# Kernel tuning notes

Measured on AMD Instinct MI355X. Metric: run time of the kernel, lower is better.

## Reference

```python
import jax, jax.numpy as jnp
import numpy as np

IN0, OUT0 = 64, 64   # layer 0: input_size -> hidden
IN1, OUT1 = 64, 16   # layer 1: hidden -> output_size
H = 2                # subnetwork hidden width (subnetwork_shape=[2,2])
BATCH = 16384


def _make_layer_params(key, n_subnets):
    ks = jax.random.split(key, 6)
    s1 = 1.0  # fan_in=1
    s2 = 1.0 / np.sqrt(H)
    W1 = jax.random.uniform(ks[0], (n_subnets, H, 1), minval=-s1, maxval=s1)
    b1 = jax.random.uniform(ks[1], (n_subnets, H), minval=-s1, maxval=s1)
    W2 = jax.random.uniform(ks[2], (n_subnets, H, H), minval=-s2, maxval=s2)
    b2 = jax.random.uniform(ks[3], (n_subnets, H), minval=-s2, maxval=s2)
    W3 = jax.random.uniform(ks[4], (n_subnets, 1, H), minval=-s2, maxval=s2)
    b3 = jax.random.uniform(ks[5], (n_subnets, 1), minval=-s2, maxval=s2)
    return W1, b1, W2, b2, W3, b3


def setup_inputs() -> dict:
    key = jax.random.key(0)
    kx, k0, k1 = jax.random.split(key, 3)
    x = jax.random.normal(kx, (BATCH, IN0), dtype=jnp.float32)
    l0 = _make_layer_params(k0, IN0 * OUT0)
    l1 = _make_layer_params(k1, IN1 * OUT1)
    names = ['W1', 'b1', 'W2', 'b2', 'W3', 'b3']
    inp = {'x': x}
    for n, v in zip(names, l0):
        inp['l0_' + n] = v
    for n, v in zip(names, l1):
        inp['l1_' + n] = v
    return inp


def _kan_layer(x, in_size, out_size, W1, b1, W2, b2, W3, b3):
    # x: [B, in] -> x_expanded: [in*out, B, 1]; subnet n = i*out + o
    B = x.shape[0]
    xe = jnp.repeat(x.T, out_size, axis=0)[:, :, None]          # [N, B, 1]
    h = jax.nn.relu(jnp.einsum('nbi,nhi->nbh', xe, W1) + b1[:, None, :])  # [N, B, H]
    h = jax.nn.relu(jnp.einsum('nbh,nkh->nbk', h, W2) + b2[:, None, :])   # [N, B, H]
    o = jnp.einsum('nbk,nok->nbo', h, W3) + b3[:, None, :]                # [N, B, 1]
    o = o[..., 0].reshape(in_size, out_size, B).sum(axis=0)               # [out, B]
    return o.T                                                            # [B, out]


def reference(x, l0_W1, l0_b1, l0_W2, l0_b2, l0_W3, l0_b3,
              l1_W1, l1_b1, l1_W2, l1_b2, l1_W3, l1_b3):
    h = _kan_layer(x, IN0, OUT0, l0_W1, l0_b1, l0_W2, l0_b2, l0_W3, l0_b3)
    out = _kan_layer(h, IN1, OUT1, l1_W1, l1_b1, l1_W2, l1_b2, l1_W3, l1_b3)
    return out
```

## Files before the change

### kernel.cpp

```cpp
#include <hip/hip_runtime.h>


typedef float v2f __attribute__((ext_vector_type(2)));

#define BATCH 16384
#define TB    32

__global__ __launch_bounds__(512, 4) void kan_fused(
    const float* __restrict__ x,
    const float* __restrict__ A1, const float* __restrict__ a1,
    const float* __restrict__ A2, const float* __restrict__ a2,
    const float* __restrict__ A3, const float* __restrict__ a3,
    const float* __restrict__ B1, const float* __restrict__ c1,
    const float* __restrict__ B2, const float* __restrict__ c2,
    const float* __restrict__ B3, const float* __restrict__ c3,
    float* __restrict__ out)
{
    __shared__ float xs[64][36];
    __shared__ float hp[4][TB][64];
    __shared__ float ht[64][36];
    __shared__ float op[4][TB][16];

    const int t    = threadIdx.x;
    const int lane = t & 63;
    const int wave = t >> 6;
    const int iq   = wave & 3;
    const int bh   = wave >> 2;
    const int bB0  = blockIdx.x * TB;

    {
        const int k = t * 4;
        const float4 v = *(const float4*)(x + (long)bB0 * 64 + k);
        const int b = k >> 6, i = k & 63;
        xs[i][b] = v.x; xs[i + 1][b] = v.y; xs[i + 2][b] = v.z; xs[i + 3][b] = v.w;
    }
    __syncthreads();

    const v2f zz = {0.f, 0.f};
    const int boff = 16 * bh;

    {
        const int o  = lane;
        const int i0 = 16 * iq;

        auto ldw = [&](int i, v2f& w1, v2f& d1, float4& w2, v2f& d2, v2f& w3, float& b3v) {
            const int n = (i << 6) + o;
            w1  = *(const v2f*)(A1 + 2 * n);
            d1  = *(const v2f*)(a1 + 2 * n);
            w2  = *(const float4*)(A2 + 4 * n);
            d2  = *(const v2f*)(a2 + 2 * n);
            w3  = *(const v2f*)(A3 + 2 * n);
            b3v = a3[n];
        };

        v2f acc[8];
#pragma unroll
        for (int j = 0; j < 8; ++j) acc[j] = zz;
        float bsum = 0.f;

        v2f w1, d1, d2, w3; float4 w2; float b3v;
        ldw(i0, w1, d1, w2, d2, w3, b3v);

#pragma unroll 1
        for (int ii = 0; ii < 16; ++ii) {
            const int i = i0 + ii;
            v2f nw1, nd1, nd2, nw3; float4 nw2; float nb3;
            ldw(i0 + ((ii + 1) & 15), nw1, nd1, nw2, nd2, nw3, nb3);

            const v2f W1X = {w1.x, w1.x}, W1Y = {w1.y, w1.y};
            const v2f D1X = {d1.x, d1.x}, D1Y = {d1.y, d1.y};
            const v2f W2X = {w2.x, w2.x}, W2Y = {w2.y, w2.y};
            const v2f W2Z = {w2.z, w2.z}, W2W = {w2.w, w2.w};
            const v2f D2X = {d2.x, d2.x}, D2Y = {d2.y, d2.y};
            const v2f W3X = {w3.x, w3.x}, W3Y = {w3.y, w3.y};

            const float4 xv0 = *(const float4*)&xs[i][boff];
            const float4 xv1 = *(const float4*)&xs[i][boff + 4];
            const float4 xv2 = *(const float4*)&xs[i][boff + 8];
            const float4 xv3 = *(const float4*)&xs[i][boff + 12];
            const float4 xq[4] = {xv0, xv1, xv2, xv3};
            const v2f* xp = (const v2f*)xq;

            bsum += b3v;
#pragma unroll
            for (int jp = 0; jp < 8; ++jp) {
                v2f m0 = __builtin_elementwise_fma(xp[jp], W1X, D1X);
                v2f m1 = __builtin_elementwise_fma(xp[jp], W1Y, D1Y);
                m0 = __builtin_elementwise_max(m0, zz);
                m1 = __builtin_elementwise_max(m1, zz);
                v2f t0 = __builtin_elementwise_fma(W2Y, m1, D2X);
                t0 = __builtin_elementwise_fma(W2X, m0, t0);
                v2f t1 = __builtin_elementwise_fma(W2W, m1, D2Y);
                t1 = __builtin_elementwise_fma(W2Z, m0, t1);
                t0 = __builtin_elementwise_max(t0, zz);
                t1 = __builtin_elementwise_max(t1, zz);
                acc[jp] = __builtin_elementwise_fma(W3X, t0, acc[jp]);
                acc[jp] = __builtin_elementwise_fma(W3Y, t1, acc[jp]);
            }
            w1 = nw1; d1 = nd1; w2 = nw2; d2 = nd2; w3 = nw3; b3v = nb3;
        }
#pragma unroll
        for (int jp = 0; jp < 8; ++jp) {
            hp[iq][boff + 2 * jp][o]     = acc[jp].x + bsum;
            hp[iq][boff + 2 * jp + 1][o] = acc[jp].y + bsum;
        }
    }
    __syncthreads();

    for (int k = t; k < TB * 64; k += 512) {
        const int b = k >> 6, i = k & 63;
        ht[i][b] = hp[0][b][i] + hp[1][b][i] + hp[2][b][i] + hp[3][b][i];
    }
    __syncthreads();

    {
        const int o1 = lane & 15;
        const int ig = lane >> 4;
        const int i0 = 16 * iq + 4 * ig;

        auto ldw = [&](int i, v2f& w1, v2f& d1, float4& w2, v2f& d2, v2f& w3, float& b3v) {
            const int n = (i << 4) + o1;
            w1  = *(const v2f*)(B1 + 2 * n);
            d1  = *(const v2f*)(c1 + 2 * n);
            w2  = *(const float4*)(B2 + 4 * n);
            d2  = *(const v2f*)(c2 + 2 * n);
            w3  = *(const v2f*)(B3 + 2 * n);
            b3v = c3[n];
        };

        v2f acc[8];
#pragma unroll
        for (int j = 0; j < 8; ++j) acc[j] = zz;
        float bsum = 0.f;

        v2f w1, d1, d2, w3; float4 w2; float b3v;
        ldw(i0, w1, d1, w2, d2, w3, b3v);

#pragma unroll 1
        for (int ii = 0; ii < 4; ++ii) {
            const int i = i0 + ii;
            v2f nw1, nd1, nd2, nw3; float4 nw2; float nb3;
            ldw(i0 + ((ii + 1) & 3), nw1, nd1, nw2, nd2, nw3, nb3);

            const v2f W1X = {w1.x, w1.x}, W1Y = {w1.y, w1.y};
            const v2f D1X = {d1.x, d1.x}, D1Y = {d1.y, d1.y};
            const v2f W2X = {w2.x, w2.x}, W2Y = {w2.y, w2.y};
            const v2f W2Z = {w2.z, w2.z}, W2W = {w2.w, w2.w};
            const v2f D2X = {d2.x, d2.x}, D2Y = {d2.y, d2.y};
            const v2f W3X = {w3.x, w3.x}, W3Y = {w3.y, w3.y};

            const float4 hv0 = *(const float4*)&ht[i][boff];
            const float4 hv1 = *(const float4*)&ht[i][boff + 4];
            const float4 hv2 = *(const float4*)&ht[i][boff + 8];
            const float4 hv3 = *(const float4*)&ht[i][boff + 12];
            const float4 hq[4] = {hv0, hv1, hv2, hv3};
            const v2f* hpair = (const v2f*)hq;

            bsum += b3v;
#pragma unroll
            for (int jp = 0; jp < 8; ++jp) {
                v2f m0 = __builtin_elementwise_fma(hpair[jp], W1X, D1X);
                v2f m1 = __builtin_elementwise_fma(hpair[jp], W1Y, D1Y);
                m0 = __builtin_elementwise_max(m0, zz);
                m1 = __builtin_elementwise_max(m1, zz);
                v2f t0 = __builtin_elementwise_fma(W2Y, m1, D2X);
                t0 = __builtin_elementwise_fma(W2X, m0, t0);
                v2f t1 = __builtin_elementwise_fma(W2W, m1, D2Y);
                t1 = __builtin_elementwise_fma(W2Z, m0, t1);
                t0 = __builtin_elementwise_max(t0, zz);
                t1 = __builtin_elementwise_max(t1, zz);
                acc[jp] = __builtin_elementwise_fma(W3X, t0, acc[jp]);
                acc[jp] = __builtin_elementwise_fma(W3Y, t1, acc[jp]);
            }
            w1 = nw1; d1 = nd1; w2 = nw2; d2 = nd2; w3 = nw3; b3v = nb3;
        }

#pragma unroll
        for (int jp = 0; jp < 8; ++jp) {
#pragma unroll
            for (int h = 0; h < 2; ++h) {
                float v = ((h == 0) ? acc[jp].x : acc[jp].y) + bsum;
                v += __shfl_xor(v, 16, 64);
                v += __shfl_xor(v, 32, 64);
                if (ig == 0) op[iq][boff + 2 * jp + h][o1] = v;
            }
        }
    }
    __syncthreads();

    if (t < 128) {
        const int f = t * 4;
        const float4 p0 = *(const float4*)(&op[0][0][0] + f);
        const float4 p1 = *(const float4*)(&op[1][0][0] + f);
        const float4 p2 = *(const float4*)(&op[2][0][0] + f);
        const float4 p3 = *(const float4*)(&op[3][0][0] + f);
        float4 r;
        r.x = p0.x + p1.x + p2.x + p3.x;
        r.y = p0.y + p1.y + p2.y + p3.y;
        r.z = p0.z + p1.z + p2.z + p3.z;
        r.w = p0.w + p1.w + p2.w + p3.w;
        *(float4*)(out + (long)bB0 * 16 + f) = r;
    }
}

extern "C" void kernel_launch(void* const* d_in, const int* in_sizes, int n_in,
                              void* d_out, int out_size, void* d_ws, size_t ws_size,
                              hipStream_t stream) {
    const float* x     = (const float*)d_in[0];
    const float* l0_W1 = (const float*)d_in[1];
    const float* l0_b1 = (const float*)d_in[2];
    const float* l0_W2 = (const float*)d_in[3];
    const float* l0_b2 = (const float*)d_in[4];
    const float* l0_W3 = (const float*)d_in[5];
    const float* l0_b3 = (const float*)d_in[6];
    const float* l1_W1 = (const float*)d_in[7];
    const float* l1_b1 = (const float*)d_in[8];
    const float* l1_W2 = (const float*)d_in[9];
    const float* l1_b2 = (const float*)d_in[10];
    const float* l1_W3 = (const float*)d_in[11];
    const float* l1_b3 = (const float*)d_in[12];

    float* outp = (float*)d_out;

    dim3 blk(512);
    dim3 grid(BATCH / TB);
    hipLaunchKernelGGL(kan_fused, grid, blk, 0, stream,
                       x,
                       l0_W1, l0_b1, l0_W2, l0_b2, l0_W3, l0_b3,
                       l1_W1, l1_b1, l1_W2, l1_b2, l1_W3, l1_b3,
                       outp);
}
```

Baseline: 103.8 us.

## Assign full input range per wave and double batch tile to drop partial-sum reductions

The batch tile grows to 64 rows per block, and each wave now owns 8 batch rows and loops over all 64 inputs, rather than splitting the input dimension across waves. This removes the shared-memory partial-sum buffers, the cross-wave reduction pass, the extra barriers, and the shuffle reduction in layer 1. Layer 1 writes results straight to global memory. In exchange, each thread does fewer batch rows per weight load, so weight loads per FLOP rise and the inner loop offers less ILP, and occupancy drops to 2 blocks per CU.

```diff
diff --git a/kernel.cpp b/kernel.cpp
--- a/kernel.cpp
+++ b/kernel.cpp
@@ -4,9 +4,9 @@
 typedef float v2f __attribute__((ext_vector_type(2)));
 
 #define BATCH 16384
-#define TB    32
+#define TB    64
 
-__global__ __launch_bounds__(512, 4) void kan_fused(
+__global__ __launch_bounds__(512, 2) void kan_fused(
     const float* __restrict__ x,
     const float* __restrict__ A1, const float* __restrict__ a1,
     const float* __restrict__ A2, const float* __restrict__ a2,
@@ -16,20 +16,17 @@
     const float* __restrict__ B3, const float* __restrict__ c3,
     float* __restrict__ out)
 {
-    __shared__ float xs[64][36];
-    __shared__ float hp[4][TB][64];
-    __shared__ float ht[64][36];
-    __shared__ float op[4][TB][16];
+    __shared__ float xs[64][68];
+    __shared__ float ht[64][68];
 
     const int t    = threadIdx.x;
     const int lane = t & 63;
     const int wave = t >> 6;
-    const int iq   = wave & 3;
-    const int bh   = wave >> 2;
+    const int boff = 8 * wave;
     const int bB0  = blockIdx.x * TB;
 
-    {
-        const int k = t * 4;
+#pragma unroll
+    for (int k = t * 4; k < TB * 64; k += 512 * 4) {
         const float4 v = *(const float4*)(x + (long)bB0 * 64 + k);
         const int b = k >> 6, i = k & 63;
         xs[i][b] = v.x; xs[i + 1][b] = v.y; xs[i + 2][b] = v.z; xs[i + 3][b] = v.w;
@@ -37,11 +34,9 @@
     __syncthreads();
 
     const v2f zz = {0.f, 0.f};
-    const int boff = 16 * bh;
 
     {
-        const int o  = lane;
-        const int i0 = 16 * iq;
+        const int o = lane;
 
         auto ldw = [&](int i, v2f& w1, v2f& d1, float4& w2, v2f& d2, v2f& w3, float& b3v) {
             const int n = (i << 6) + o;
@@ -53,19 +48,18 @@
             b3v = a3[n];
         };
 
-        v2f acc[8];
+        v2f acc[4];
 #pragma unroll
-        for (int j = 0; j < 8; ++j) acc[j] = zz;
+        for (int j = 0; j < 4; ++j) acc[j] = zz;
         float bsum = 0.f;
 
         v2f w1, d1, d2, w3; float4 w2; float b3v;
-        ldw(i0, w1, d1, w2, d2, w3, b3v);
+        ldw(0, w1, d1, w2, d2, w3, b3v);
 
 #pragma unroll 1
-        for (int ii = 0; ii < 16; ++ii) {
-            const int i = i0 + ii;
+        for (int ii = 0; ii < 64; ++ii) {
             v2f nw1, nd1, nd2, nw3; float4 nw2; float nb3;
-            ldw(i0 + ((ii + 1) & 15), nw1, nd1, nw2, nd2, nw3, nb3);
+            ldw((ii + 1) & 63, nw1, nd1, nw2, nd2, nw3, nb3);
 
             const v2f W1X = {w1.x, w1.x}, W1Y = {w1.y, w1.y};
             const v2f D1X = {d1.x, d1.x}, D1Y = {d1.y, d1.y};
@@ -74,16 +68,14 @@
             const v2f D2X = {d2.x, d2.x}, D2Y = {d2.y, d2.y};
             const v2f W3X = {w3.x, w3.x}, W3Y = {w3.y, w3.y};
 
-            const float4 xv0 = *(const float4*)&xs[i][boff];
-            const float4 xv1 = *(const float4*)&xs[i][boff + 4];
-            const float4 xv2 = *(const float4*)&xs[i][boff + 8];
-            const float4 xv3 = *(const float4*)&xs[i][boff + 12];
-            const float4 xq[4] = {xv0, xv1, xv2, xv3};
+            const float4 xv0 = *(const float4*)&xs[ii][boff];
+            const float4 xv1 = *(const float4*)&xs[ii][boff + 4];
+            const float4 xq[2] = {xv0, xv1};
             const v2f* xp = (const v2f*)xq;
 
             bsum += b3v;
 #pragma unroll
-            for (int jp = 0; jp < 8; ++jp) {
+            for (int jp = 0; jp < 4; ++jp) {
                 v2f m0 = __builtin_elementwise_fma(xp[jp], W1X, D1X);
                 v2f m1 = __builtin_elementwise_fma(xp[jp], W1Y, D1Y);
                 m0 = __builtin_elementwise_max(m0, zz);
@@ -100,23 +92,17 @@
             w1 = nw1; d1 = nd1; w2 = nw2; d2 = nd2; w3 = nw3; b3v = nb3;
         }
 #pragma unroll
-        for (int jp = 0; jp < 8; ++jp) {
-            hp[iq][boff + 2 * jp][o]     = acc[jp].x + bsum;
-            hp[iq][boff + 2 * jp + 1][o] = acc[jp].y + bsum;
+        for (int jp = 0; jp < 4; ++jp) {
+            ht[o][boff + 2 * jp]     = acc[jp].x + bsum;
+            ht[o][boff + 2 * jp + 1] = acc[jp].y + bsum;
         }
-    }
-    __syncthreads();
-
-    for (int k = t; k < TB * 64; k += 512) {
-        const int b = k >> 6, i = k & 63;
-        ht[i][b] = hp[0][b][i] + hp[1][b][i] + hp[2][b][i] + hp[3][b][i];
     }
     __syncthreads();
 
     {
         const int o1 = lane & 15;
-        const int ig = lane >> 4;
-        const int i0 = 16 * iq + 4 * ig;
+        const int bg = lane >> 4;
+        const int bp = boff + 2 * bg;
 
         auto ldw = [&](int i, v2f& w1, v2f& d1, float4& w2, v2f& d2, v2f& w3, float& b3v) {
             const int n = (i << 4) + o1;
@@ -128,19 +114,16 @@
             b3v = c3[n];
         };
 
-        v2f acc[8];
-#pragma unroll
-        for (int j = 0; j < 8; ++j) acc[j] = zz;
+        v2f accA = zz, accB = zz;
         float bsum = 0.f;
 
         v2f w1, d1, d2, w3; float4 w2; float b3v;
-        ldw(i0, w1, d1, w2, d2, w3, b3v);
+        ldw(0, w1, d1, w2, d2, w3, b3v);
 
 #pragma unroll 1
-        for (int ii = 0; ii < 4; ++ii) {
-            const int i = i0 + ii;
+        for (int ii = 0; ii < 64; ++ii) {
             v2f nw1, nd1, nd2, nw3; float4 nw2; float nb3;
-            ldw(i0 + ((ii + 1) & 3), nw1, nd1, nw2, nd2, nw3, nb3);
+            ldw((ii + 1) & 63, nw1, nd1, nw2, nd2, nw3, nb3);
 
             const v2f W1X = {w1.x, w1.x}, W1Y = {w1.y, w1.y};
             const v2f D1X = {d1.x, d1.x}, D1Y = {d1.y, d1.y};
@@ -149,57 +132,32 @@
             const v2f D2X = {d2.x, d2.x}, D2Y = {d2.y, d2.y};
             const v2f W3X = {w3.x, w3.x}, W3Y = {w3.y, w3.y};
 
-            const float4 hv0 = *(const float4*)&ht[i][boff];
-            const float4 hv1 = *(const float4*)&ht[i][boff + 4];
-            const float4 hv2 = *(const float4*)&ht[i][boff + 8];
-            const float4 hv3 = *(const float4*)&ht[i][boff + 12];
-            const float4 hq[4] = {hv0, hv1, hv2, hv3};
-            const v2f* hpair = (const v2f*)hq;
+            const v2f hv = *(const v2f*)&ht[ii][bp];
 
             bsum += b3v;
-#pragma unroll
-            for (int jp = 0; jp < 8; ++jp) {
-                v2f m0 = __builtin_elementwise_fma(hpair[jp], W1X, D1X);
-                v2f m1 = __builtin_elementwise_fma(hpair[jp], W1Y, D1Y);
-                m0 = __builtin_elementwise_max(m0, zz);
-                m1 = __builtin_elementwise_max(m1, zz);
-                v2f t0 = __builtin_elementwise_fma(W2Y, m1, D2X);
-                t0 = __builtin_elementwise_fma(W2X, m0, t0);
-                v2f t1 = __builtin_elementwise_fma(W2W, m1, D2Y);
-                t1 = __builtin_elementwise_fma(W2Z, m0, t1);
-                t0 = __builtin_elementwise_max(t0, zz);
-                t1 = __builtin_elementwise_max(t1, zz);
-                acc[jp] = __builtin_elementwise_fma(W3X, t0, acc[jp]);
-                acc[jp] = __builtin_elementwise_fma(W3Y, t1, acc[jp]);
+            v2f m0 = __builtin_elementwise_fma(hv, W1X, D1X);
+            v2f m1 = __builtin_elementwise_fma(hv, W1Y, D1Y);
+            m0 = __builtin_elementwise_max(m0, zz);
+            m1 = __builtin_elementwise_max(m1, zz);
+            v2f t0 = __builtin_elementwise_fma(W2Y, m1, D2X);
+            t0 = __builtin_elementwise_fma(W2X, m0, t0);
+            v2f t1 = __builtin_elementwise_fma(W2W, m1, D2Y);
+            t1 = __builtin_elementwise_fma(W2Z, m0, t1);
+            t0 = __builtin_elementwise_max(t0, zz);
+            t1 = __builtin_elementwise_max(t1, zz);
+            if (ii & 1) {
+                accB = __builtin_elementwise_fma(W3X, t0, accB);
+                accB = __builtin_elementwise_fma(W3Y, t1, accB);
+            } else {
+                accA = __builtin_elementwise_fma(W3X, t0, accA);
+                accA = __builtin_elementwise_fma(W3Y, t1, accA);
             }
             w1 = nw1; d1 = nd1; w2 = nw2; d2 = nd2; w3 = nw3; b3v = nb3;
         }
 
-#pragma unroll
-        for (int jp = 0; jp < 8; ++jp) {
-#pragma unroll
-            for (int h = 0; h < 2; ++h) {
-                float v = ((h == 0) ? acc[jp].x : acc[jp].y) + bsum;
-                v += __shfl_xor(v, 16, 64);
-                v += __shfl_xor(v, 32, 64);
-                if (ig == 0) op[iq][boff + 2 * jp + h][o1] = v;
-            }
-        }
-    }
-    __syncthreads();
-
-    if (t < 128) {
-        const int f = t * 4;
-        const float4 p0 = *(const float4*)(&op[0][0][0] + f);
-        const float4 p1 = *(const float4*)(&op[1][0][0] + f);
-        const float4 p2 = *(const float4*)(&op[2][0][0] + f);
-        const float4 p3 = *(const float4*)(&op[3][0][0] + f);
-        float4 r;
-        r.x = p0.x + p1.x + p2.x + p3.x;
-        r.y = p0.y + p1.y + p2.y + p3.y;
-        r.z = p0.z + p1.z + p2.z + p3.z;
-        r.w = p0.w + p1.w + p2.w + p3.w;
-        *(float4*)(out + (long)bB0 * 16 + f) = r;
+        const v2f r = accA + accB;
+        out[(long)(bB0 + bp) * 16 + o1]     = r.x + bsum;
+        out[(long)(bB0 + bp + 1) * 16 + o1] = r.y + bsum;
     }
 }
 
```

Result: slower. 131.7 us (+26.9%).
